# Kernel tuning notes

Hardware: AMD Instinct MI355X
Metric: run time of the kernel (lower is better)

Reference implementation:

```python
import jax, jax.numpy as jnp
import numpy as np

G, NPG, EPG = 128, 256, 4096   # graphs, nodes/graph, edges/graph
N, E = G * NPG, G * EPG
IN, H = 64, 64
RATIO = 0.5
K = int(RATIO * EPG)  # edges reserved per graph


def setup_inputs() -> dict:
    key = jax.random.key(0)
    ks = jax.random.split(key, 20)
    x = jax.random.normal(ks[0], (N, IN), dtype=jnp.float32)
    # per-graph random edges (block-diagonal structure, contiguous per graph)
    src = jax.random.randint(ks[1], (G, EPG), 0, NPG)
    dst = jax.random.randint(ks[2], (G, EPG), 0, NPG)
    offs = (jnp.arange(G) * NPG)[:, None]
    edge_index = jnp.stack([(src + offs).reshape(-1), (dst + offs).reshape(-1)]).astype(jnp.int64)
    edge_attr = jax.random.uniform(ks[3], (E,), dtype=jnp.float32)
    batch = jnp.repeat(jnp.arange(G), NPG).astype(jnp.int64)

    def w(k, shape):
        return jax.random.normal(k, shape, dtype=jnp.float32) * 0.1
    return {
        'x': x, 'edge_attr': edge_attr,
        'W11': w(ks[4], (H, IN)), 'b11': w(ks[5], (H,)), 'W12': w(ks[6], (H, IN)),
        'W13': w(ks[7], (H, IN)), 'b13': w(ks[8], (H,)),
        'W21': w(ks[9], (H, H)), 'b21': w(ks[10], (H,)), 'W22': w(ks[11], (H, H)),
        'W23': w(ks[12], (H, H)), 'b23': w(ks[13], (H,)),
        'Wm1': w(ks[14], (4 * H, 2 * H)), 'bm1': w(ks[15], (4 * H,)),
        'Wm2': w(ks[16], (1, 4 * H)), 'bm2': w(ks[17], (1,)),
        'edge_index': edge_index, 'batch': batch,
    }


def leconv(x, row, col, ew, W1, b1, W2, W3, b3):
    # PyG LEConv: out_i = sum_{(j->i)} e_ji * (lin1(x_j) - lin2(x_i)) + lin3(x_i)
    a = x @ W1.T + b1          # lin1 (bias)
    b = x @ W2.T               # lin2 (no bias)
    msg = ew[:, None] * (a[row] - b[col])            # [E, H]
    agg = jax.ops.segment_sum(msg, col, num_segments=x.shape[0])
    return agg + x @ W3.T + b3


def relabel_edges(ei):
    # torch relabel(): map used nodes to compact ids; fixed-shape variant returns
    # the remapped edge_index plus a node-presence mask instead of gathering x.
    present = jnp.zeros((N,), jnp.int32).at[ei.reshape(-1)].set(1)
    nid = jnp.where(present == 1, jnp.cumsum(present) - 1, -1)
    return nid[ei], present


def reference(x, edge_attr, W11, b11, W12, W13, b13, W21, b21, W22, W23, b23,
              Wm1, bm1, Wm2, bm2, edge_index, batch):
    row, col = edge_index[0], edge_index[1]
    h = jax.nn.relu(leconv(x, row, col, edge_attr, W11, b11, W12, W13, b13))
    h = leconv(h, row, col, edge_attr, W21, b21, W22, W23, b23)
    # edge scoring MLP on concat(x[row], x[col])
    edge_rep = jnp.concatenate([h[row], h[col]], axis=-1)       # [E, 2H]
    score = (jax.nn.relu(edge_rep @ Wm1.T + bm1) @ Wm2.T + bm2).reshape(-1)  # [E]
    # per-graph top-k split (graphs are uniform -> static shapes)
    s = score.reshape(G, EPG)
    order = jnp.argsort(-s, axis=1)
    keep, drop = order[:, :K], order[:, K:]
    causal_w = jnp.take_along_axis(s, keep, axis=1).reshape(-1)
    conf_w = -jnp.take_along_axis(s, drop, axis=1).reshape(-1)
    eoffs = (jnp.arange(G) * EPG)[:, None]
    kg = (keep + eoffs).reshape(-1)
    dg = (drop + eoffs).reshape(-1)
    causal_ei = edge_index[:, kg]
    conf_ei = edge_index[:, dg]
    causal_ei_rel, causal_mask = relabel_edges(causal_ei)
    conf_ei_rel, conf_mask = relabel_edges(conf_ei)
    out = jnp.concatenate([score, causal_w, conf_w])            # [2E]
    return out, causal_ei_rel, conf_ei_rel, causal_mask, conf_mask
```

## Files before the change

### kernel.cpp

```cpp
#include <hip/hip_runtime.h>
#include <cstddef>

#define G_    128
#define NPG_  256
#define EPG_  4096
#define NN_   32768
#define EE_   524288
#define KK_   2048
#define GK_   262144

#define O_CW  524288
#define O_DW  786432
#define O_CEI 1048576
#define O_FEI 1572864
#define O_CM  2097152
#define O_DM  2129920

typedef float v4f __attribute__((ext_vector_type(4)));
typedef unsigned long long u64;

struct BiasCfg {
  const float* b[8];
};

__device__ __forceinline__ void cswap(u64& a, u64& b, bool d) {
  u64 hi = a > b ? a : b, lo = a > b ? b : a;
  a = d ? hi : lo;
  b = d ? lo : hi;
}

__device__ __forceinline__ void gemm_wt_body(const float* __restrict__ in, int istride,
                                             const float* __restrict__ WT, int wstride,
                                             const BiasCfg& bc, int ncb,
                                             float* __restrict__ out, int ostride,
                                             int bx, float* xT) {
  const int tid = threadIdx.x;
  const int r0 = bx * 64;
#pragma unroll
  for (int it = 0; it < 16; ++it) {
    int idx = tid + it * 256;
    int rr = idx >> 6, kk = idx & 63;
    xT[kk * 68 + rr] = in[(r0 + rr) * istride + kk];
  }
  __syncthreads();
  const int c4 = (tid & 15) * 4;
  const int r4 = (tid >> 4) * 4;
  for (int cb = 0; cb < ncb; ++cb) {
    const float* wp = WT + cb * 64 + c4;
    const float* bp = bc.b[cb];
    float acc[4][4] = {};
#pragma unroll
    for (int k = 0; k < 64; ++k) {
      float4 xv = *(const float4*)&xT[k * 68 + r4];
      float4 wv = *(const float4*)&wp[(size_t)k * wstride];
      float xr[4] = {xv.x, xv.y, xv.z, xv.w};
      float wc[4] = {wv.x, wv.y, wv.z, wv.w};
#pragma unroll
      for (int a = 0; a < 4; ++a)
#pragma unroll
        for (int b = 0; b < 4; ++b)
          acc[a][b] = fmaf(xr[a], wc[b], acc[a][b]);
    }
    float bx4[4] = {0.f, 0.f, 0.f, 0.f};
    if (bp) {
      float4 bb = *(const float4*)&bp[c4];
      bx4[0] = bb.x; bx4[1] = bb.y; bx4[2] = bb.z; bx4[3] = bb.w;
    }
#pragma unroll
    for (int ri = 0; ri < 4; ++ri) {
      v4f st;
      st.x = acc[ri][0] + bx4[0];
      st.y = acc[ri][1] + bx4[1];
      st.z = acc[ri][2] + bx4[2];
      st.w = acc[ri][3] + bx4[3];
      __builtin_nontemporal_store(st, (v4f*)&out[(r0 + r4 + ri) * ostride + cb * 64 + c4]);
    }
    __syncthreads();
  }
}

__global__ __launch_bounds__(256, 4) void gemm_wt(const float* __restrict__ in, int istride,
                                                  const float* __restrict__ WT, int wstride,
                                                  BiasCfg bc, int ncb,
                                                  float* __restrict__ out, int ostride) {
  __shared__ float xT[64 * 68];
  gemm_wt_body(in, istride, WT, wstride, bc, ncb, out, ostride, blockIdx.x, xT);
}

__global__ __launch_bounds__(256) void prep_kernel(const float* __restrict__ Wm1,
                                                   const float* __restrict__ W11, const float* __restrict__ W12,
                                                   const float* __restrict__ W13,
                                                   const float* __restrict__ W21, const float* __restrict__ W22,
                                                   const float* __restrict__ W23,
                                                   float* __restrict__ WmT, float* __restrict__ W1T,
                                                   float* __restrict__ W2T, int* __restrict__ masks) {
  const int b = blockIdx.x;
  const int tid = threadIdx.x;
  if (b < 64) {
    const int k = b;
#pragma unroll
    for (int t = 0; t < 2; ++t) {
      int j = t * 256 + tid;
      int row = j & 255;
      int koff = (j < 256) ? 0 : 64;
      WmT[k * 512 + j] = Wm1[row * 128 + koff + k];
    }
  } else if (b < 80) {
    const int kb = (b - 64) * 4;
    if (tid < 192) {
      int cb = tid >> 6, c = tid & 63;
      const float* Wsrc = (cb == 0) ? W11 : (cb == 1) ? W12 : W13;
#pragma unroll
      for (int s = 0; s < 4; ++s) {
        int k = kb + s;
        W1T[k * 192 + tid] = Wsrc[c * 64 + k];
      }
    }
  } else if (b < 96) {
    const int kb = (b - 80) * 4;
    if (tid < 192) {
      int cb = tid >> 6, c = tid & 63;
      const float* Wsrc = (cb == 0) ? W21 : (cb == 1) ? W22 : W23;
#pragma unroll
      for (int s = 0; s < 4; ++s) {
        int k = kb + s;
        W2T[k * 192 + tid] = Wsrc[c * 64 + k];
      }
    }
  } else {
    int idx = (b - 96) * 1024 + tid * 4;
    int4 z = {0, 0, 0, 0};
    *(int4*)&masks[idx] = z;
  }
}

__global__ __launch_bounds__(256) void build_dense(const int* __restrict__ ei, const float* __restrict__ ea,
                                                   float* __restrict__ MT, float* __restrict__ Wc) {
  __shared__ float acc[NPG_ * 128];
  const int tid = threadIdx.x;
  const int g = blockIdx.x >> 1;
  const int c0 = (blockIdx.x & 1) * 128;
  const int gbase = g * NPG_;
  const size_t mbase = (size_t)g << 16;
  for (int i = tid * 4; i < NPG_ * 128; i += 1024) {
    float4 z = {0.f, 0.f, 0.f, 0.f};
    *(float4*)&acc[i] = z;
  }
  __syncthreads();
  const int ebase = g * EPG_;
#pragma unroll
  for (int it = 0; it < 16; ++it) {
    int e = ebase + it * 256 + tid;
    int r = ei[e] - gbase;
    int ch = ei[EE_ + e] - gbase - c0;
    float w = ea[e];
    if ((unsigned)ch < 128u) atomicAdd(&acc[r * 128 + ch], w);
  }
  __syncthreads();
  for (int i = tid; i < NPG_ * 32; i += 256) {
    int r = i >> 5, c4 = (i & 31) * 4;
    *(float4*)&MT[mbase + (size_t)r * 256 + c0 + c4] = *(const float4*)&acc[r * 128 + c4];
  }
  if (tid < 128) {
    float s = 0.f;
    for (int r = 0; r < NPG_; ++r) s += acc[r * 128 + tid];
    Wc[gbase + c0 + tid] = s;
  }
}

__global__ __launch_bounds__(256) void mm_agg(const float* __restrict__ MT, const float* __restrict__ buf,
                                              const float* __restrict__ Wc, float* __restrict__ hout,
                                              int do_relu) {
  __shared__ float Ms[64 * 72];
  __shared__ float As[64 * 72];
  const int tid = threadIdx.x;
  const int g = blockIdx.x >> 2;
  const int c0 = (blockIdx.x & 3) * 64;
  const int gbase = g * NPG_;
  const size_t mbase = (size_t)g << 16;
  const int c4 = (tid >> 4) * 4;
  const int k4 = (tid & 15) * 4;
  float acc[4][4] = {};
  for (int kc = 0; kc < 4; ++kc) {
#pragma unroll
    for (int it = 0; it < 4; ++it) {
      int idx = tid + it * 256;
      int rr = idx >> 4, c16 = (idx & 15) * 4;
      *(float4*)&Ms[rr * 72 + c16] = *(const float4*)&MT[mbase + (size_t)(kc * 64 + rr) * 256 + c0 + c16];
      *(float4*)&As[rr * 72 + c16] = *(const float4*)&buf[(gbase + kc * 64 + rr) * 192 + c16];
    }
    __syncthreads();
#pragma unroll
    for (int r = 0; r < 64; ++r) {
      float4 mv = *(const float4*)&Ms[r * 72 + c4];
      float4 av = *(const float4*)&As[r * 72 + k4];
      float mr[4] = {mv.x, mv.y, mv.z, mv.w};
      float ak[4] = {av.x, av.y, av.z, av.w};
#pragma unroll
      for (int ci = 0; ci < 4; ++ci)
#pragma unroll
        for (int ki = 0; ki < 4; ++ki)
          acc[ci][ki] = fmaf(mr[ci], ak[ki], acc[ci][ki]);
    }
    __syncthreads();
  }
#pragma unroll
  for (int ci = 0; ci < 4; ++ci) {
    int n = gbase + c0 + c4 + ci;
    float wcn = Wc[n];
    float4 b4 = *(const float4*)&buf[n * 192 + 64 + k4];
    float4 cc4 = *(const float4*)&buf[n * 192 + 128 + k4];
    float4 st;
    st.x = acc[ci][0] - wcn * b4.x + cc4.x;
    st.y = acc[ci][1] - wcn * b4.y + cc4.y;
    st.z = acc[ci][2] - wcn * b4.z + cc4.z;
    st.w = acc[ci][3] - wcn * b4.w + cc4.w;
    if (do_relu) {
      st.x = fmaxf(st.x, 0.f); st.y = fmaxf(st.y, 0.f);
      st.z = fmaxf(st.z, 0.f); st.w = fmaxf(st.w, 0.f);
    }
    *(float4*)&hout[n * 64 + k4] = st;
  }
}

__global__ __launch_bounds__(256, 4) void score_v5(const float* __restrict__ pq, const int* __restrict__ ei,
                                                   const float* __restrict__ wm2, const float* __restrict__ bm2,
                                                   float* __restrict__ out) {
  __shared__ float Ps[256 * 20];
  __shared__ float Qs[256 * 20];
  const int tid = threadIdx.x;
  const int g = blockIdx.x & 127;
  const int eighth = blockIdx.x >> 7;
  const int gbase = g * NPG_;
  const int ebase = g * EPG_ + eighth * 512;
  int rl[2], cl[2];
  float acc[2] = {};
#pragma unroll
  for (int j = 0; j < 2; ++j) {
    int e = ebase + j * 256 + tid;
    rl[j] = (ei[e] - gbase) * 20;
    cl[j] = (ei[EE_ + e] - gbase) * 20;
  }
  for (int t = 0; t < 16; ++t) {
    __syncthreads();
#pragma unroll
    for (int it = 0; it < 4; ++it) {
      int idx = tid + it * 256;
      int node = idx >> 2, k4 = (idx & 3) * 4;
      const float* src = &pq[(size_t)(gbase + node) * 512 + t * 16 + k4];
      *(float4*)&Ps[node * 20 + k4] = *(const float4*)src;
      *(float4*)&Qs[node * 20 + k4] = *(const float4*)(src + 256);
    }
    __syncthreads();
#pragma unroll
    for (int k4 = 0; k4 < 16; k4 += 4) {
      float4 w4 = *(const float4*)&wm2[t * 16 + k4];
#pragma unroll
      for (int j = 0; j < 2; ++j) {
        float4 p = *(const float4*)&Ps[rl[j] + k4];
        float4 q = *(const float4*)&Qs[cl[j] + k4];
        acc[j] = fmaf(w4.x, fmaxf(p.x + q.x, 0.f), acc[j]);
        acc[j] = fmaf(w4.y, fmaxf(p.y + q.y, 0.f), acc[j]);
        acc[j] = fmaf(w4.z, fmaxf(p.z + q.z, 0.f), acc[j]);
        acc[j] = fmaf(w4.w, fmaxf(p.w + q.w, 0.f), acc[j]);
      }
    }
  }
  const float beta = bm2[0];
#pragma unroll
  for (int j = 0; j < 2; ++j) out[ebase + j * 256 + tid] = acc[j] + beta;
}

__global__ __launch_bounds__(1024) void sort_kernel(float* __restrict__ out, const int* __restrict__ ei,
                                                    int* __restrict__ kg, int* __restrict__ dg,
                                                    int* __restrict__ cmask, int* __restrict__ dmask) {
  __shared__ u64 keys[EPG_];
  const int g = blockIdx.x;
  const int tid = threadIdx.x;
  const int b = 4 * tid;
  u64 e[4];
  {
    float4 s4 = *(const float4*)&out[g * EPG_ + b];
    float sv[4] = {s4.x, s4.y, s4.z, s4.w};
#pragma unroll
    for (int s = 0; s < 4; ++s) {
      unsigned u = __float_as_uint(sv[s]);
      u = (u & 0x80000000u) ? ~u : (u | 0x80000000u);
      e[s] = ((u64)u << 32) | (unsigned)(~(b + s));
    }
  }
  cswap(e[0], e[1], true);
  cswap(e[2], e[3], false);
  {
    bool d = ((b & 4) == 0);
    cswap(e[0], e[2], d); cswap(e[1], e[3], d);
    cswap(e[0], e[1], d); cswap(e[2], e[3], d);
  }
  for (int k = 8; k <= EPG_; k <<= 1) {
    if (k >= 512) {
#pragma unroll
      for (int s = 0; s < 4; ++s) keys[b + s] = e[s];
      __syncthreads();
      for (int j = k >> 1; j >= 256; j >>= 1) {
        const int jm1 = j - 1;
        const int p0 = tid, p1 = tid + 1024;
        const int i0 = ((p0 & ~jm1) << 1) | (p0 & jm1);
        const int i1 = ((p1 & ~jm1) << 1) | (p1 & jm1);
        u64 a0 = keys[i0], b0 = keys[i0 + j];
        u64 a1 = keys[i1], b1 = keys[i1 + j];
        bool d0 = ((i0 & k) == 0), d1 = ((i1 & k) == 0);
        u64 hi0 = a0 > b0 ? a0 : b0, lo0 = a0 > b0 ? b0 : a0;
        u64 hi1 = a1 > b1 ? a1 : b1, lo1 = a1 > b1 ? b1 : a1;
        keys[i0]     = d0 ? hi0 : lo0;
        keys[i0 + j] = d0 ? lo0 : hi0;
        keys[i1]     = d1 ? hi1 : lo1;
        keys[i1 + j] = d1 ? lo1 : hi1;
        __syncthreads();
      }
#pragma unroll
      for (int s = 0; s < 4; ++s) e[s] = keys[b + s];
    }
    const bool d = ((tid & (k >> 2)) == 0);
    for (int j = (k >> 1) > 128 ? 128 : (k >> 1); j >= 4; j >>= 1) {
      const int delta = j >> 2;
      const bool lower = ((tid & delta) == 0);
      const bool keepmax = (lower == d);
#pragma unroll
      for (int s = 0; s < 4; ++s) {
        u64 p = __shfl_xor(e[s], delta);
        u64 mx = e[s] > p ? e[s] : p;
        u64 mn = e[s] > p ? p : e[s];
        e[s] = keepmax ? mx : mn;
      }
    }
    cswap(e[0], e[2], d); cswap(e[1], e[3], d);
    cswap(e[0], e[1], d); cswap(e[2], e[3], d);
  }
#pragma unroll
  for (int s = 0; s < 4; ++s) {
    const int p = b + s;
    u64 kv = e[s];
    int i = (int)(~(unsigned)kv);
    unsigned hi = (unsigned)(kv >> 32);
    unsigned ub = (hi & 0x80000000u) ? (hi ^ 0x80000000u) : ~hi;
    float sc = __uint_as_float(ub);
    int ed = g * EPG_ + i;
    int r = ei[ed], c = ei[EE_ + ed];
    if (p < KK_) {
      out[O_CW + g * KK_ + p] = sc;
      kg[g * KK_ + p] = ed;
      cmask[r] = 1; cmask[c] = 1;
    } else {
      int q = p - KK_;
      out[O_DW + g * KK_ + q] = -sc;
      dg[g * KK_ + q] = ed;
      dmask[r] = 1; dmask[c] = 1;
    }
  }
}

__global__ __launch_bounds__(1024) void scan_kernel(const int* __restrict__ masks, int* __restrict__ nids) {
  const int which = blockIdx.x;
  const int* m = masks + which * NN_;
  int* nid = nids + which * NN_;
  const int tid = threadIdx.x;
  const int base = tid * 32;
  int local[32];
  int sum = 0;
#pragma unroll
  for (int j = 0; j < 32; ++j) { local[j] = m[base + j]; sum += local[j]; }
  __shared__ int ps[1024];
  ps[tid] = sum;
  __syncthreads();
  for (int off = 1; off < 1024; off <<= 1) {
    int v = (tid >= off) ? ps[tid - off] : 0;
    __syncthreads();
    ps[tid] += v;
    __syncthreads();
  }
  int run = ps[tid] - sum;
#pragma unroll
  for (int j = 0; j < 32; ++j) { run += local[j]; nid[base + j] = run - 1; }
}

__global__ __launch_bounds__(256) void finalize_kernel(const int* __restrict__ kg, const int* __restrict__ dg,
                                                       const int* __restrict__ ei,
                                                       const int* __restrict__ nid_c, const int* __restrict__ nid_d,
                                                       const int* __restrict__ cmask, const int* __restrict__ dmask,
                                                       float* __restrict__ out) {
  const int p = blockIdx.x * 256 + threadIdx.x;
  int e = kg[p];
  out[O_CEI + p]       = (float)nid_c[ei[e]];
  out[O_CEI + GK_ + p] = (float)nid_c[ei[EE_ + e]];
  int e2 = dg[p];
  out[O_FEI + p]       = (float)nid_d[ei[e2]];
  out[O_FEI + GK_ + p] = (float)nid_d[ei[EE_ + e2]];
  if (p < NN_) {
    out[O_CM + p] = (float)cmask[p];
    out[O_DM + p] = (float)dmask[p];
  }
}

extern "C" void kernel_launch(void* const* d_in, const int* in_sizes, int n_in,
                              void* d_out, int out_size, void* d_ws, size_t ws_size,
                              hipStream_t stream) {
  (void)in_sizes; (void)n_in; (void)out_size; (void)ws_size;
  const float* x   = (const float*)d_in[0];
  const float* ea  = (const float*)d_in[1];
  const float* W11 = (const float*)d_in[2];
  const float* b11 = (const float*)d_in[3];
  const float* W12 = (const float*)d_in[4];
  const float* W13 = (const float*)d_in[5];
  const float* b13 = (const float*)d_in[6];
  const float* W21 = (const float*)d_in[7];
  const float* b21 = (const float*)d_in[8];
  const float* W22 = (const float*)d_in[9];
  const float* W23 = (const float*)d_in[10];
  const float* b23 = (const float*)d_in[11];
  const float* Wm1 = (const float*)d_in[12];
  const float* bm1 = (const float*)d_in[13];
  const float* Wm2 = (const float*)d_in[14];
  const float* bm2 = (const float*)d_in[15];
  const int*   ei  = (const int*)d_in[16];
  float* out = (float*)d_out;
  float* ws  = (float*)d_ws;

  float* MT  = ws;
  float* Wc  = ws + 8388608;
  float* buf = ws + 8421376;
  float* pq  = ws;
  float* h_c = ws + 16777216;
  int* kg    = (int*)(ws + 18874368);
  int* dg    = kg + GK_;
  int* cmask = dg + GK_;
  int* dmask = cmask + NN_;
  int* nid_c = dmask + NN_;
  int* nid_d = nid_c + NN_;
  float* WmT = ws + 18874368;
  float* W1T = WmT + 32768;
  float* W2T = W1T + 12288;

  prep_kernel<<<160, 256, 0, stream>>>(Wm1, W11, W12, W13, W21, W22, W23, WmT, W1T, W2T, cmask);

  build_dense<<<256, 256, 0, stream>>>(ei, ea, MT, Wc);

  BiasCfg bc1{};
  bc1.b[0] = b11; bc1.b[1] = nullptr; bc1.b[2] = b13;
  gemm_wt<<<512, 256, 0, stream>>>(x, 64, W1T, 192, bc1, 3, buf, 192);

  mm_agg<<<512, 256, 0, stream>>>(MT, buf, Wc, h_c, 1);

  BiasCfg bc2{};
  bc2.b[0] = b21; bc2.b[1] = nullptr; bc2.b[2] = b23;
  gemm_wt<<<512, 256, 0, stream>>>(h_c, 64, W2T, 192, bc2, 3, buf, 192);

  mm_agg<<<512, 256, 0, stream>>>(MT, buf, Wc, h_c, 0);

  BiasCfg bc3{};
  for (int cb = 0; cb < 4; ++cb) { bc3.b[cb] = bm1 + cb * 64; bc3.b[cb + 4] = nullptr; }
  gemm_wt<<<512, 256, 0, stream>>>(h_c, 64, WmT, 512, bc3, 8, pq, 512);

  score_v5<<<1024, 256, 0, stream>>>(pq, ei, Wm2, bm2, out);

  sort_kernel<<<G_, 1024, 0, stream>>>(out, ei, kg, dg, cmask, dmask);

  scan_kernel<<<2, 1024, 0, stream>>>(cmask, nid_c);

  finalize_kernel<<<GK_ / 256, 256, 0, stream>>>(kg, dg, ei, nid_c, nid_d, cmask, dmask, out);
}
```

Before: 329.0 us.

## Rewrite edge scoring to gather P/Q rows directly with 16-lane edge groups

```diff
diff --git a/kernel.cpp b/kernel.cpp
--- a/kernel.cpp
+++ b/kernel.cpp
@@ -223,52 +223,77 @@
   }
 }
 
-__global__ __launch_bounds__(256, 4) void score_v5(const float* __restrict__ pq, const int* __restrict__ ei,
+struct EdgeRegs { float4 p0, p1, p2, p3, q0, q1, q2, q3; };
+
+__device__ __forceinline__ void load_edge(const float* __restrict__ pq, int r, int c, int s, EdgeRegs& R) {
+  const float4* Pp = (const float4*)(pq + (size_t)r * 512) + s;
+  const float4* Qp = (const float4*)(pq + (size_t)c * 512 + 256) + s;
+  R.p0 = Pp[0];  R.p1 = Pp[16]; R.p2 = Pp[32]; R.p3 = Pp[48];
+  R.q0 = Qp[0];  R.q1 = Qp[16]; R.q2 = Qp[32]; R.q3 = Qp[48];
+}
+
+#define ACC4(A, W, P, Q)                                  \
+  A = fmaf(W.x, fmaxf(P.x + Q.x, 0.f), A);                \
+  A = fmaf(W.y, fmaxf(P.y + Q.y, 0.f), A);                \
+  A = fmaf(W.z, fmaxf(P.z + Q.z, 0.f), A);                \
+  A = fmaf(W.w, fmaxf(P.w + Q.w, 0.f), A);
+
+__device__ __forceinline__ float edge_score(const EdgeRegs& R, float4 w0, float4 w1, float4 w2, float4 w3) {
+  float a0 = 0.f, a1 = 0.f;
+  ACC4(a0, w0, R.p0, R.q0);
+  ACC4(a1, w1, R.p1, R.q1);
+  ACC4(a0, w2, R.p2, R.q2);
+  ACC4(a1, w3, R.p3, R.q3);
+  return a0 + a1;
+}
+
+__global__ __launch_bounds__(256, 4) void score_v6(const float* __restrict__ pq, const int* __restrict__ ei,
                                                    const float* __restrict__ wm2, const float* __restrict__ bm2,
                                                    float* __restrict__ out) {
-  __shared__ float Ps[256 * 20];
-  __shared__ float Qs[256 * 20];
+  __shared__ float sbuf[512];
   const int tid = threadIdx.x;
   const int g = blockIdx.x & 127;
   const int eighth = blockIdx.x >> 7;
-  const int gbase = g * NPG_;
   const int ebase = g * EPG_ + eighth * 512;
-  int rl[2], cl[2];
-  float acc[2] = {};
-#pragma unroll
-  for (int j = 0; j < 2; ++j) {
-    int e = ebase + j * 256 + tid;
-    rl[j] = (ei[e] - gbase) * 20;
-    cl[j] = (ei[EE_ + e] - gbase) * 20;
-  }
-  for (int t = 0; t < 16; ++t) {
-    __syncthreads();
-#pragma unroll
-    for (int it = 0; it < 4; ++it) {
-      int idx = tid + it * 256;
-      int node = idx >> 2, k4 = (idx & 3) * 4;
-      const float* src = &pq[(size_t)(gbase + node) * 512 + t * 16 + k4];
-      *(float4*)&Ps[node * 20 + k4] = *(const float4*)src;
-      *(float4*)&Qs[node * 20 + k4] = *(const float4*)(src + 256);
-    }
-    __syncthreads();
-#pragma unroll
-    for (int k4 = 0; k4 < 16; k4 += 4) {
-      float4 w4 = *(const float4*)&wm2[t * 16 + k4];
-#pragma unroll
-      for (int j = 0; j < 2; ++j) {
-        float4 p = *(const float4*)&Ps[rl[j] + k4];
-        float4 q = *(const float4*)&Qs[cl[j] + k4];
-        acc[j] = fmaf(w4.x, fmaxf(p.x + q.x, 0.f), acc[j]);
-        acc[j] = fmaf(w4.y, fmaxf(p.y + q.y, 0.f), acc[j]);
-        acc[j] = fmaf(w4.z, fmaxf(p.z + q.z, 0.f), acc[j]);
-        acc[j] = fmaf(w4.w, fmaxf(p.w + q.w, 0.f), acc[j]);
-      }
-    }
-  }
+  const int slot = tid >> 4;
+  const int s = tid & 15;
+  const float4 w0 = *(const float4*)&wm2[s * 4];
+  const float4 w1 = *(const float4*)&wm2[64 + s * 4];
+  const float4 w2 = *(const float4*)&wm2[128 + s * 4];
+  const float4 w3 = *(const float4*)&wm2[192 + s * 4];
   const float beta = bm2[0];
-#pragma unroll
-  for (int j = 0; j < 2; ++j) out[ebase + j * 256 + tid] = acc[j] + beta;
+  const int e0 = ebase + slot * 32;
+
+  EdgeRegs A, B;
+  {
+    int r = ei[e0], c = ei[EE_ + e0];
+    load_edge(pq, r, c, s, A);
+  }
+#pragma unroll 1
+  for (int n = 0; n < 32; n += 2) {
+    {
+      int e1 = e0 + n + 1;
+      int r = ei[e1], c = ei[EE_ + e1];
+      load_edge(pq, r, c, s, B);
+    }
+    float a = edge_score(A, w0, w1, w2, w3);
+    a += __shfl_xor(a, 1); a += __shfl_xor(a, 2);
+    a += __shfl_xor(a, 4); a += __shfl_xor(a, 8);
+    if (s == 0) sbuf[slot * 32 + n] = a;
+    if (n + 2 < 32) {
+      int e2 = e0 + n + 2;
+      int r = ei[e2], c = ei[EE_ + e2];
+      load_edge(pq, r, c, s, A);
+    }
+    float b = edge_score(B, w0, w1, w2, w3);
+    b += __shfl_xor(b, 1); b += __shfl_xor(b, 2);
+    b += __shfl_xor(b, 4); b += __shfl_xor(b, 8);
+    if (s == 0) sbuf[slot * 32 + n + 1] = b;
+  }
+  __syncthreads();
+  float2 v = *(const float2*)&sbuf[tid * 2];
+  v.x += beta; v.y += beta;
+  *(float2*)&out[ebase + tid * 2] = v;
 }
 
 __global__ __launch_bounds__(1024) void sort_kernel(float* __restrict__ out, const int* __restrict__ ei,
@@ -460,7 +485,7 @@
   for (int cb = 0; cb < 4; ++cb) { bc3.b[cb] = bm1 + cb * 64; bc3.b[cb + 4] = nullptr; }
   gemm_wt<<<512, 256, 0, stream>>>(h_c, 64, WmT, 512, bc3, 8, pq, 512);
 
-  score_v5<<<1024, 256, 0, stream>>>(pq, ei, Wm2, bm2, out);
+  score_v6<<<1024, 256, 0, stream>>>(pq, ei, Wm2, bm2, out);
 
   sort_kernel<<<G_, 1024, 0, stream>>>(out, ei, kg, dg, cmask, dmask);
 
```

Result: slower. 368.9 us (+12.1%).

## Sort edges by source node in-block and read score operands directly from global

Applied to the files above, without the earlier changes.

```diff
diff --git a/kernel.cpp b/kernel.cpp
--- a/kernel.cpp
+++ b/kernel.cpp
@@ -223,52 +223,98 @@
   }
 }
 
-__global__ __launch_bounds__(256, 4) void score_v5(const float* __restrict__ pq, const int* __restrict__ ei,
-                                                   const float* __restrict__ wm2, const float* __restrict__ bm2,
-                                                   float* __restrict__ out) {
-  __shared__ float Ps[256 * 20];
-  __shared__ float Qs[256 * 20];
+__global__ __launch_bounds__(512, 2) void score_v11(const float* __restrict__ pq, const int* __restrict__ ei,
+                                                    const float* __restrict__ wm2, const float* __restrict__ bm2,
+                                                    float* __restrict__ out) {
+  __shared__ int sorted_[1024];
+  __shared__ int hist_[256];
+  __shared__ int off_[256];
+  __shared__ int cur_[256];
+  __shared__ int wsum_[4];
   const int tid = threadIdx.x;
   const int g = blockIdx.x & 127;
-  const int eighth = blockIdx.x >> 7;
+  const int quarter = blockIdx.x >> 7;
   const int gbase = g * NPG_;
-  const int ebase = g * EPG_ + eighth * 512;
-  int rl[2], cl[2];
+  const int ebase = g * EPG_ + quarter * 1024;
+  if (tid < 256) { hist_[tid] = 0; cur_[tid] = 0; }
+  int rr[2], cc[2];
+#pragma unroll
+  for (int j = 0; j < 2; ++j) {
+    int e = ebase + j * 512 + tid;
+    rr[j] = ei[e] - gbase;
+    cc[j] = ei[EE_ + e] - gbase;
+  }
+  __syncthreads();
+#pragma unroll
+  for (int j = 0; j < 2; ++j) atomicAdd(&hist_[rr[j]], 1);
+  __syncthreads();
+  int sv = 0, vv = 0;
+  if (tid < 256) {
+    const int l = tid & 63;
+    vv = hist_[tid];
+    sv = vv;
+#pragma unroll
+    for (int d = 1; d < 64; d <<= 1) {
+      int u = __shfl_up(sv, d);
+      if (l >= d) sv += u;
+    }
+    if (l == 63) wsum_[tid >> 6] = sv;
+  }
+  __syncthreads();
+  if (tid < 256) {
+    const int w = tid >> 6;
+    int woff = 0;
+#pragma unroll
+    for (int ww = 0; ww < 3; ++ww)
+      if (ww < w) woff += wsum_[ww];
+    off_[tid] = woff + sv - vv;
+  }
+  __syncthreads();
+#pragma unroll
+  for (int j = 0; j < 2; ++j) {
+    int pos = off_[rr[j]] + atomicAdd(&cur_[rr[j]], 1);
+    sorted_[pos] = (rr[j] << 18) | (cc[j] << 10) | (j * 512 + tid);
+  }
+  __syncthreads();
+  const float* rp0; const float* rp1; const float* qp0; const float* qp1;
+  int eo[2];
+  {
+    int rec0 = sorted_[tid];
+    int rec1 = sorted_[512 + tid];
+    rp0 = pq + (size_t)(gbase + (rec0 >> 18)) * 512;
+    qp0 = pq + (size_t)(gbase + ((rec0 >> 10) & 255)) * 512 + 256;
+    eo[0] = ebase + (rec0 & 1023);
+    rp1 = pq + (size_t)(gbase + (rec1 >> 18)) * 512;
+    qp1 = pq + (size_t)(gbase + ((rec1 >> 10) & 255)) * 512 + 256;
+    eo[1] = ebase + (rec1 & 1023);
+  }
   float acc[2] = {};
-#pragma unroll
-  for (int j = 0; j < 2; ++j) {
-    int e = ebase + j * 256 + tid;
-    rl[j] = (ei[e] - gbase) * 20;
-    cl[j] = (ei[EE_ + e] - gbase) * 20;
-  }
   for (int t = 0; t < 16; ++t) {
     __syncthreads();
-#pragma unroll
-    for (int it = 0; it < 4; ++it) {
-      int idx = tid + it * 256;
-      int node = idx >> 2, k4 = (idx & 3) * 4;
-      const float* src = &pq[(size_t)(gbase + node) * 512 + t * 16 + k4];
-      *(float4*)&Ps[node * 20 + k4] = *(const float4*)src;
-      *(float4*)&Qs[node * 20 + k4] = *(const float4*)(src + 256);
-    }
-    __syncthreads();
-#pragma unroll
-    for (int k4 = 0; k4 < 16; k4 += 4) {
-      float4 w4 = *(const float4*)&wm2[t * 16 + k4];
-#pragma unroll
-      for (int j = 0; j < 2; ++j) {
-        float4 p = *(const float4*)&Ps[rl[j] + k4];
-        float4 q = *(const float4*)&Qs[cl[j] + k4];
-        acc[j] = fmaf(w4.x, fmaxf(p.x + q.x, 0.f), acc[j]);
-        acc[j] = fmaf(w4.y, fmaxf(p.y + q.y, 0.f), acc[j]);
-        acc[j] = fmaf(w4.z, fmaxf(p.z + q.z, 0.f), acc[j]);
-        acc[j] = fmaf(w4.w, fmaxf(p.w + q.w, 0.f), acc[j]);
-      }
+    const float* P0 = rp0 + t * 16;
+    const float* Q0 = qp0 + t * 16;
+    const float* P1 = rp1 + t * 16;
+    const float* Q1 = qp1 + t * 16;
+#pragma unroll
+    for (int k4 = 0; k4 < 4; ++k4) {
+      float4 w4 = *(const float4*)&wm2[t * 16 + k4 * 4];
+      float4 p0 = *(const float4*)(P0 + k4 * 4);
+      float4 q0 = *(const float4*)(Q0 + k4 * 4);
+      float4 p1 = *(const float4*)(P1 + k4 * 4);
+      float4 q1 = *(const float4*)(Q1 + k4 * 4);
+      acc[0] = fmaf(w4.x, fmaxf(p0.x + q0.x, 0.f), acc[0]);
+      acc[0] = fmaf(w4.y, fmaxf(p0.y + q0.y, 0.f), acc[0]);
+      acc[0] = fmaf(w4.z, fmaxf(p0.z + q0.z, 0.f), acc[0]);
+      acc[0] = fmaf(w4.w, fmaxf(p0.w + q0.w, 0.f), acc[0]);
+      acc[1] = fmaf(w4.x, fmaxf(p1.x + q1.x, 0.f), acc[1]);
+      acc[1] = fmaf(w4.y, fmaxf(p1.y + q1.y, 0.f), acc[1]);
+      acc[1] = fmaf(w4.z, fmaxf(p1.z + q1.z, 0.f), acc[1]);
+      acc[1] = fmaf(w4.w, fmaxf(p1.w + q1.w, 0.f), acc[1]);
     }
   }
   const float beta = bm2[0];
-#pragma unroll
-  for (int j = 0; j < 2; ++j) out[ebase + j * 256 + tid] = acc[j] + beta;
+  out[eo[0]] = acc[0] + beta;
+  out[eo[1]] = acc[1] + beta;
 }
 
 __global__ __launch_bounds__(1024) void sort_kernel(float* __restrict__ out, const int* __restrict__ ei,
@@ -460,7 +506,7 @@
   for (int cb = 0; cb < 4; ++cb) { bc3.b[cb] = bm1 + cb * 64; bc3.b[cb + 4] = nullptr; }
   gemm_wt<<<512, 256, 0, stream>>>(h_c, 64, WmT, 512, bc3, 8, pq, 512);
 
-  score_v5<<<1024, 256, 0, stream>>>(pq, ei, Wm2, bm2, out);
+  score_v11<<<512, 512, 0, stream>>>(pq, ei, Wm2, bm2, out);
 
   sort_kernel<<<G_, 1024, 0, stream>>>(out, ei, kg, dg, cmask, dmask);
 
```

Result: slower. 385.5 us (+17.2%).
